# Kernel tuning notes

Hardware: AMD Instinct MI355X
Metric: run time of the kernel (lower is better)

Reference implementation:

```python
import jax, jax.numpy as jnp
import numpy as np

N_NODES = 100000
N_EDGES = 3200000
IN_C, HID_C, OUT_C = 5, 128, 64


def setup_inputs() -> dict:
    key = jax.random.key(0)
    k_x, k_e, k_w1, k_b1, k_w2, k_b2 = jax.random.split(key, 6)
    x = jax.random.normal(k_x, (N_NODES, IN_C), dtype=jnp.float32)
    edge_index = jax.random.randint(k_e, (2, N_EDGES), 0, N_NODES, dtype=jnp.int32)
    # GCNConv learned params (glorot weights, zero-ish bias)
    W1 = jax.random.normal(k_w1, (IN_C, HID_C), dtype=jnp.float32) * (1.0 / np.sqrt(IN_C))
    b1 = jax.random.normal(k_b1, (HID_C,), dtype=jnp.float32) * 0.01
    W2 = jax.random.normal(k_w2, (HID_C, OUT_C), dtype=jnp.float32) * (1.0 / np.sqrt(HID_C))
    b2 = jax.random.normal(k_b2, (OUT_C,), dtype=jnp.float32) * 0.01
    return {"x": x, "edge_index": edge_index, "W1": W1, "b1": b1, "W2": W2, "b2": b2}


def _gcn_conv(x, src, dst, deg_inv_sqrt, W, b):
    """One GCNConv (PyG defaults: self-loops already in src/dst, symmetric norm, bias)."""
    h = x @ W                                   # [N, C_out]
    norm = deg_inv_sqrt[src] * deg_inv_sqrt[dst]  # [E+N]
    msg = h[src] * norm[:, None]                # gather + scale
    out = jax.ops.segment_sum(msg, dst, num_segments=x.shape[0])  # scatter-add
    return out + b


def reference(x, edge_index, W1, b1, W2, b2):
    n = x.shape[0]
    loop = jnp.arange(n, dtype=edge_index.dtype)
    src = jnp.concatenate([edge_index[0], loop])  # self-loops appended
    dst = jnp.concatenate([edge_index[1], loop])
    deg = jax.ops.segment_sum(jnp.ones_like(src, dtype=x.dtype), dst, num_segments=n)
    deg_inv_sqrt = jnp.where(deg > 0, jax.lax.rsqrt(deg), 0.0)
    h = _gcn_conv(x, src, dst, deg_inv_sqrt, W1, b1)
    z = _gcn_conv(h, src, dst, deg_inv_sqrt, W2, b2)
    return z
```

## Files before the change

### kernel.cpp

```cpp
#include <hip/hip_runtime.h>

#define IN_C  5
#define HID_C 128
#define OUT_C 64

#define KB   256
#define NBP  512
#define CAP  10240
#define TILE 8192
#define BTH  512
#define EPT  (TILE / BTH)
#define EPTV (TILE / BTH / 4)
#define GNODES 64

typedef int      vi4 __attribute__((ext_vector_type(4)));
typedef float    vf4 __attribute__((ext_vector_type(4)));
typedef _Float16 vh8 __attribute__((ext_vector_type(8)));


__global__ __launch_bounds__(BTH) void k_bin(const int* __restrict__ src,
                                             const int* __restrict__ dstp,
                                             int* __restrict__ gcursor,
                                             int* __restrict__ binned, int e) {
    __shared__ int lhist[NBP];
    __shared__ int lgofs[NBP];
    __shared__ int lbeg[NBP];
    __shared__ int lsort[TILE];
    __shared__ int gdst[TILE];
    __shared__ int wsum[8];
    __shared__ int stot;
    int tid = threadIdx.x;
    int lane = tid & 63, w = tid >> 6;
    int tbeg = blockIdx.x * TILE;
    lhist[tid] = 0;
    __syncthreads();
    int pk[EPT], bk[EPT], rk[EPT];
    #pragma unroll
    for (int q = 0; q < EPTV; ++q) {
        int idx = tbeg + (q * BTH + tid) * 4;
        if (idx < e) {
            vi4 s4 = __builtin_nontemporal_load((const vi4*)(src + idx));
            vi4 d4 = __builtin_nontemporal_load((const vi4*)(dstp + idx));
            pk[q*4+0] = ((d4.x & 255) << 24) | s4.x; bk[q*4+0] = ((unsigned)d4.x) >> 8;
            pk[q*4+1] = ((d4.y & 255) << 24) | s4.y; bk[q*4+1] = ((unsigned)d4.y) >> 8;
            pk[q*4+2] = ((d4.z & 255) << 24) | s4.z; bk[q*4+2] = ((unsigned)d4.z) >> 8;
            pk[q*4+3] = ((d4.w & 255) << 24) | s4.w; bk[q*4+3] = ((unsigned)d4.w) >> 8;
            rk[q*4+0] = atomicAdd(&lhist[bk[q*4+0]], 1);
            rk[q*4+1] = atomicAdd(&lhist[bk[q*4+1]], 1);
            rk[q*4+2] = atomicAdd(&lhist[bk[q*4+2]], 1);
            rk[q*4+3] = atomicAdd(&lhist[bk[q*4+3]], 1);
        } else {
            bk[q*4+0] = -1; bk[q*4+1] = -1; bk[q*4+2] = -1; bk[q*4+3] = -1;
        }
    }
    __syncthreads();
    int h = lhist[tid];
    int v = h;
    #pragma unroll
    for (int m = 1; m < 64; m <<= 1) { int u = __shfl_up(v, m); if (lane >= m) v += u; }
    if (lane == 63) wsum[w] = v;
    __syncthreads();
    if (tid == 0) {
        int s = 0;
        #pragma unroll
        for (int k = 0; k < 8; ++k) { int tv = wsum[k]; wsum[k] = s; s += tv; }
    }
    __syncthreads();
    int excl = wsum[w] + v - h;
    lbeg[tid] = excl;
    if (h > 0)
        lgofs[tid] = tid * CAP + atomicAdd(&gcursor[tid], h) - excl;
    if (tid == BTH - 1) stot = excl + h;
    __syncthreads();
    #pragma unroll
    for (int q = 0; q < EPT; ++q) {
        if (bk[q] >= 0) {
            int slot = lbeg[bk[q]] + rk[q];
            lsort[slot] = pk[q];
            gdst[slot] = lgofs[bk[q]] + slot;
        }
    }
    __syncthreads();
    int tot = stot;
    for (int i = tid; i < tot; i += BTH)
        binned[gdst[i]] = lsort[i];
}

__global__ __launch_bounds__(BTH) void k_build(int* __restrict__ binned,
                                               const int* __restrict__ gcursor,
                                               const float* __restrict__ x,
                                               int2* __restrict__ pse,
                                               _Float16* __restrict__ xs, int n) {
    __shared__ int cnt[KB];
    __shared__ int wt[4];
    __shared__ int wte[4];
    __shared__ int stage[CAP];
    int tid = threadIdx.x;
    int lane = tid & 63, w = tid >> 6;
    int bkt = blockIdx.x;
    int beg = bkt * CAP;
    int tot = gcursor[bkt];
    if (tid < KB) cnt[tid] = 0;
    __syncthreads();
    int4 r[5];
    int4 rr[5];
    #pragma unroll
    for (int it = 0; it < 5; ++it) {
        int j0 = (tid << 2) + it * (BTH * 4);
        if (j0 < tot) {
            r[it] = *(const int4*)(binned + beg + j0);
            rr[it].x = atomicAdd(&cnt[((unsigned)r[it].x) >> 24], 1);
            if (j0 + 1 < tot) rr[it].y = atomicAdd(&cnt[((unsigned)r[it].y) >> 24], 1);
            if (j0 + 2 < tot) rr[it].z = atomicAdd(&cnt[((unsigned)r[it].z) >> 24], 1);
            if (j0 + 3 < tot) rr[it].w = atomicAdd(&cnt[((unsigned)r[it].w) >> 24], 1);
        }
    }
    __syncthreads();
    int deg = (tid < KB) ? cnt[tid] : 0;
    int v = deg;
    #pragma unroll
    for (int m = 1; m < 64; m <<= 1) { int u = __shfl_up(v, m); if (lane >= m) v += u; }
    if (tid < KB && lane == 63) wt[w] = v;
    __syncthreads();
    if (tid == 0) {
        int s = 0;
        #pragma unroll
        for (int k = 0; k < 4; ++k) { wte[k] = s; s += wt[k]; }
    }
    __syncthreads();
    if (tid < KB) {
        int rel = wte[w] + v - deg;
        int node = bkt * KB + tid;
        pse[node] = make_int2(beg + rel, beg + rel + deg);
        cnt[tid] = rel;
        float d = rsqrtf(1.0f + (float)deg);
        vh8 hq = {};
        if (node < n) {
            hq[0] = (_Float16)(x[node * IN_C + 0] * d);
            hq[1] = (_Float16)(x[node * IN_C + 1] * d);
            hq[2] = (_Float16)(x[node * IN_C + 2] * d);
            hq[3] = (_Float16)(x[node * IN_C + 3] * d);
            hq[4] = (_Float16)(x[node * IN_C + 4] * d);
            hq[5] = (_Float16)d;
        }
        *((vh8*)(xs + (size_t)node * 8)) = hq;
    }
    __syncthreads();
    #pragma unroll
    for (int it = 0; it < 5; ++it) {
        int j0 = (tid << 2) + it * (BTH * 4);
        if (j0 < tot) {
            stage[cnt[((unsigned)r[it].x) >> 24] + rr[it].x] = r[it].x & 0xFFFFFF;
            if (j0 + 1 < tot)
                stage[cnt[((unsigned)r[it].y) >> 24] + rr[it].y] = r[it].y & 0xFFFFFF;
            if (j0 + 2 < tot)
                stage[cnt[((unsigned)r[it].z) >> 24] + rr[it].z] = r[it].z & 0xFFFFFF;
            if (j0 + 3 < tot)
                stage[cnt[((unsigned)r[it].w) >> 24] + rr[it].w] = r[it].w & 0xFFFFFF;
        }
    }
    __syncthreads();
    for (int j = tid; j < tot; j += BTH)
        binned[beg + j] = stage[j];
}

__global__ __launch_bounds__(BTH) void k_gath0(const int* __restrict__ srclist,
                                               const int2* __restrict__ pse,
                                               const _Float16* __restrict__ feat,
                                               _Float16* __restrict__ outf,
                                               float* __restrict__ tout, int n) {
    int tid = threadIdx.x;
    int node = blockIdx.x * GNODES + (tid >> 3);
    int sub = tid & 7;
    if (node >= n) return;
    int2 pp = pse[node];
    int ps = pp.x, pe = pp.y;
    float a0 = 0, a1 = 0, a2 = 0, a3 = 0, a4 = 0, a5 = 0;
    int j = ps + sub;
    for (; j + 24 < pe; j += 32) {
        int s0 = srclist[j],      s1 = srclist[j + 8];
        int s2 = srclist[j + 16], s3 = srclist[j + 24];
        vh8 h0 = *(const vh8*)(feat + (size_t)s0 * 8);
        vh8 h1 = *(const vh8*)(feat + (size_t)s1 * 8);
        vh8 h2 = *(const vh8*)(feat + (size_t)s2 * 8);
        vh8 h3 = *(const vh8*)(feat + (size_t)s3 * 8);
        a0 += ((float)h0[0] + (float)h1[0]) + ((float)h2[0] + (float)h3[0]);
        a1 += ((float)h0[1] + (float)h1[1]) + ((float)h2[1] + (float)h3[1]);
        a2 += ((float)h0[2] + (float)h1[2]) + ((float)h2[2] + (float)h3[2]);
        a3 += ((float)h0[3] + (float)h1[3]) + ((float)h2[3] + (float)h3[3]);
        a4 += ((float)h0[4] + (float)h1[4]) + ((float)h2[4] + (float)h3[4]);
        a5 += ((float)h0[5] + (float)h1[5]) + ((float)h2[5] + (float)h3[5]);
    }
    for (; j < pe; j += 8) {
        int sA = srclist[j];
        vh8 hA = *(const vh8*)(feat + (size_t)sA * 8);
        a0 += (float)hA[0]; a1 += (float)hA[1]; a2 += (float)hA[2];
        a3 += (float)hA[3]; a4 += (float)hA[4]; a5 += (float)hA[5];
    }
    #pragma unroll
    for (int m = 1; m < 8; m <<= 1) {
        a0 += __shfl_xor(a0, m);
        a1 += __shfl_xor(a1, m);
        a2 += __shfl_xor(a2, m);
        a3 += __shfl_xor(a3, m);
        a4 += __shfl_xor(a4, m);
        a5 += __shfl_xor(a5, m);
    }
    if (sub == 0) {
        vh8 hs = *(const vh8*)(feat + (size_t)node * 8);
        float d = (float)hs[5];
        a0 += (float)hs[0]; a1 += (float)hs[1]; a2 += (float)hs[2];
        a3 += (float)hs[3]; a4 += (float)hs[4]; a5 += d;
        float d2 = d * d;
        vh8 ho = {};
        ho[0] = (_Float16)(d2 * a0);
        ho[1] = (_Float16)(d2 * a1);
        ho[2] = (_Float16)(d2 * a2);
        ho[3] = (_Float16)(d2 * a3);
        ho[4] = (_Float16)(d2 * a4);
        ho[5] = (_Float16)d;
        tout[node] = d * a5;
        *((vh8*)(outf + (size_t)node * 8)) = ho;
    }
}

__global__ __launch_bounds__(BTH) void k_gout(const int* __restrict__ srclist,
                                              const int2* __restrict__ pse,
                                              const _Float16* __restrict__ feat,
                                              const float* __restrict__ t,
                                              const float* __restrict__ W1,
                                              const float* __restrict__ b1,
                                              const float* __restrict__ W2,
                                              const float* __restrict__ b2,
                                              float* __restrict__ out, int n) {
    __shared__ float snode[GNODES * 8];
    __shared__ float sW[IN_C * OUT_C + 2 * OUT_C];
    int tid = threadIdx.x;
    if (tid < IN_C * OUT_C) {
        int k = tid >> 6, c = tid & 63;
        float acc = 0.0f;
        for (int m = 0; m < HID_C; ++m)
            acc += W1[k * HID_C + m] * W2[m * OUT_C + c];
        sW[tid] = acc;
    } else if (tid < IN_C * OUT_C + OUT_C) {
        int c = tid - IN_C * OUT_C;
        float acc = 0.0f;
        for (int m = 0; m < HID_C; ++m)
            acc += b1[m] * W2[m * OUT_C + c];
        sW[tid] = acc;
    } else if (tid < IN_C * OUT_C + 2 * OUT_C) {
        sW[tid] = b2[tid - IN_C * OUT_C - OUT_C];
    }
    int node = blockIdx.x * GNODES + (tid >> 3);
    int sub = tid & 7;
    bool act = (node < n);
    float a0 = 0, a1 = 0, a2 = 0, a3 = 0, a4 = 0;
    if (act) {
        int2 pp = pse[node];
        int ps = pp.x, pe = pp.y;
        int j = ps + sub;
        for (; j + 24 < pe; j += 32) {
            int s0 = srclist[j],      s1 = srclist[j + 8];
            int s2 = srclist[j + 16], s3 = srclist[j + 24];
            vh8 h0 = *(const vh8*)(feat + (size_t)s0 * 8);
            vh8 h1 = *(const vh8*)(feat + (size_t)s1 * 8);
            vh8 h2 = *(const vh8*)(feat + (size_t)s2 * 8);
            vh8 h3 = *(const vh8*)(feat + (size_t)s3 * 8);
            a0 += ((float)h0[0] + (float)h1[0]) + ((float)h2[0] + (float)h3[0]);
            a1 += ((float)h0[1] + (float)h1[1]) + ((float)h2[1] + (float)h3[1]);
            a2 += ((float)h0[2] + (float)h1[2]) + ((float)h2[2] + (float)h3[2]);
            a3 += ((float)h0[3] + (float)h1[3]) + ((float)h2[3] + (float)h3[3]);
            a4 += ((float)h0[4] + (float)h1[4]) + ((float)h2[4] + (float)h3[4]);
        }
        for (; j < pe; j += 8) {
            int sA = srclist[j];
            vh8 hA = *(const vh8*)(feat + (size_t)sA * 8);
            a0 += (float)hA[0]; a1 += (float)hA[1]; a2 += (float)hA[2];
            a3 += (float)hA[3]; a4 += (float)hA[4];
        }
    }
    #pragma unroll
    for (int m = 1; m < 8; m <<= 1) {
        a0 += __shfl_xor(a0, m);
        a1 += __shfl_xor(a1, m);
        a2 += __shfl_xor(a2, m);
        a3 += __shfl_xor(a3, m);
        a4 += __shfl_xor(a4, m);
    }
    if (act && sub == 0) {
        vh8 hs = *(const vh8*)(feat + (size_t)node * 8);
        float d = (float)hs[5];
        a0 += (float)hs[0]; a1 += (float)hs[1]; a2 += (float)hs[2];
        a3 += (float)hs[3]; a4 += (float)hs[4];
        float* sn = snode + (tid >> 3) * 8;
        sn[0] = d * a0; sn[1] = d * a1; sn[2] = d * a2;
        sn[3] = d * a3; sn[4] = d * a4; sn[5] = t[node];
    }
    __syncthreads();
    int base = blockIdx.x * GNODES;
    for (int u = tid; u < GNODES * 16; u += BTH) {
        int ln = u >> 4, q = u & 15;
        int i = base + ln;
        if (i >= n) continue;
        const float* a = snode + ln * 8;
        float ti = a[5];
        float4 acc = ((const float4*)(sW + IN_C * OUT_C + OUT_C))[q];
        float4 bq  = ((const float4*)(sW + IN_C * OUT_C))[q];
        acc.x += ti * bq.x; acc.y += ti * bq.y;
        acc.z += ti * bq.z; acc.w += ti * bq.w;
        #pragma unroll
        for (int k = 0; k < IN_C; ++k) {
            float ak = a[k];
            float4 wk = ((const float4*)(sW + k * OUT_C))[q];
            acc.x += ak * wk.x; acc.y += ak * wk.y;
            acc.z += ak * wk.z; acc.w += ak * wk.w;
        }
        vf4 av; av.x = acc.x; av.y = acc.y; av.z = acc.z; av.w = acc.w;
        __builtin_nontemporal_store(av, ((vf4*)out) + (size_t)i * 16 + q);
    }
}

extern "C" void kernel_launch(void* const* d_in, const int* in_sizes, int n_in,
                              void* d_out, int out_size, void* d_ws, size_t ws_size,
                              hipStream_t stream) {
    const float* x   = (const float*)d_in[0];
    const int*   ei  = (const int*)d_in[1];
    const float* W1  = (const float*)d_in[2];
    const float* b1  = (const float*)d_in[3];
    const float* W2  = (const float*)d_in[4];
    const float* b2  = (const float*)d_in[5];
    float* out = (float*)d_out;

    const int n = in_sizes[0] / IN_C;
    const int e = in_sizes[1] / 2;
    const int* src = ei;
    const int* dst = ei + e;
    const int NB = (n + KB - 1) / KB;
    const int NKB = NB * KB;

    int*      gcursor = (int*)d_ws;
    int*      binned  = gcursor + 512;
    int2*     pse     = (int2*)(binned + (size_t)NBP * CAP);
    _Float16* xs      = (_Float16*)(pse + NKB);
    _Float16* p1      = xs + (size_t)8 * NKB;
    float*    t       = (float*)(p1 + (size_t)8 * NKB);

    const int gB = (e + TILE - 1) / TILE;
    const int gG = (n + GNODES - 1) / GNODES;

    (void)hipMemsetAsync(gcursor, 0, NBP * sizeof(int), stream);
    k_bin   <<<gB, BTH, 0, stream>>>(src, dst, gcursor, binned, e);
    k_build <<<NB, BTH, 0, stream>>>(binned, gcursor, x, pse, xs, n);
    k_gath0 <<<gG, BTH, 0, stream>>>(binned, pse, xs, p1, t, n);
    k_gout  <<<gG, BTH, 0, stream>>>(binned, pse, p1, t,
                                     W1, b1, W2, b2, out, n);
}
```

Baseline: 165.9 us.

## Pad per-node edge lists to multiples of four and vectorize index loads

The sort kernel now rounds each node's segment length up to a multiple of four when computing offsets, so every CSR segment starts 16-byte aligned, and it writes the sorted bucket back with int4 stores. Both gather kernels then read four source indices per int4 load, with each of the eight lanes taking contiguous groups of four and the remainder handled in a single tail step. The aim is fewer, wider index loads in the memory-bound gathers, at the cost of padding slots (stage contents at the pads are never read) and relying on the bucket capacity absorbing the extra padding.

```diff
diff --git a/kernel.cpp b/kernel.cpp
--- a/kernel.cpp
+++ b/kernel.cpp
@@ -117,7 +117,8 @@
     }
     __syncthreads();
     int deg = (tid < KB) ? cnt[tid] : 0;
-    int v = deg;
+    int pdeg = (deg + 3) & ~3;
+    int v = pdeg;
     #pragma unroll
     for (int m = 1; m < 64; m <<= 1) { int u = __shfl_up(v, m); if (lane >= m) v += u; }
     if (tid < KB && lane == 63) wt[w] = v;
@@ -129,7 +130,7 @@
     }
     __syncthreads();
     if (tid < KB) {
-        int rel = wte[w] + v - deg;
+        int rel = wte[w] + v - pdeg;
         int node = bkt * KB + tid;
         pse[node] = make_int2(beg + rel, beg + rel + deg);
         cnt[tid] = rel;
@@ -160,8 +161,13 @@
         }
     }
     __syncthreads();
-    for (int j = tid; j < tot; j += BTH)
-        binned[beg + j] = stage[j];
+    int ptot = wte[3] + wt[3];
+    for (int j4 = tid << 2; j4 < ptot; j4 += BTH * 4) {
+        int4 vq;
+        vq.x = stage[j4];     vq.y = stage[j4 + 1];
+        vq.z = stage[j4 + 2]; vq.w = stage[j4 + 3];
+        *(int4*)(binned + beg + j4) = vq;
+    }
 }
 
 __global__ __launch_bounds__(BTH) void k_gath0(const int* __restrict__ srclist,
@@ -175,15 +181,15 @@
     if (node >= n) return;
     int2 pp = pse[node];
     int ps = pp.x, pe = pp.y;
+    int deg = pe - ps;
+    int G = deg >> 2;
     float a0 = 0, a1 = 0, a2 = 0, a3 = 0, a4 = 0, a5 = 0;
-    int j = ps + sub;
-    for (; j + 24 < pe; j += 32) {
-        int s0 = srclist[j],      s1 = srclist[j + 8];
-        int s2 = srclist[j + 16], s3 = srclist[j + 24];
-        vh8 h0 = *(const vh8*)(feat + (size_t)s0 * 8);
-        vh8 h1 = *(const vh8*)(feat + (size_t)s1 * 8);
-        vh8 h2 = *(const vh8*)(feat + (size_t)s2 * 8);
-        vh8 h3 = *(const vh8*)(feat + (size_t)s3 * 8);
+    for (int i = sub; i < G; i += 8) {
+        int4 s4 = *(const int4*)(srclist + ps + (i << 2));
+        vh8 h0 = *(const vh8*)(feat + (size_t)s4.x * 8);
+        vh8 h1 = *(const vh8*)(feat + (size_t)s4.y * 8);
+        vh8 h2 = *(const vh8*)(feat + (size_t)s4.z * 8);
+        vh8 h3 = *(const vh8*)(feat + (size_t)s4.w * 8);
         a0 += ((float)h0[0] + (float)h1[0]) + ((float)h2[0] + (float)h3[0]);
         a1 += ((float)h0[1] + (float)h1[1]) + ((float)h2[1] + (float)h3[1]);
         a2 += ((float)h0[2] + (float)h1[2]) + ((float)h2[2] + (float)h3[2]);
@@ -191,8 +197,8 @@
         a4 += ((float)h0[4] + (float)h1[4]) + ((float)h2[4] + (float)h3[4]);
         a5 += ((float)h0[5] + (float)h1[5]) + ((float)h2[5] + (float)h3[5]);
     }
-    for (; j < pe; j += 8) {
-        int sA = srclist[j];
+    if (sub < (deg & 3)) {
+        int sA = srclist[ps + (G << 2) + sub];
         vh8 hA = *(const vh8*)(feat + (size_t)sA * 8);
         a0 += (float)hA[0]; a1 += (float)hA[1]; a2 += (float)hA[2];
         a3 += (float)hA[3]; a4 += (float)hA[4]; a5 += (float)hA[5];
@@ -258,22 +264,22 @@
     if (act) {
         int2 pp = pse[node];
         int ps = pp.x, pe = pp.y;
-        int j = ps + sub;
-        for (; j + 24 < pe; j += 32) {
-            int s0 = srclist[j],      s1 = srclist[j + 8];
-            int s2 = srclist[j + 16], s3 = srclist[j + 24];
-            vh8 h0 = *(const vh8*)(feat + (size_t)s0 * 8);
-            vh8 h1 = *(const vh8*)(feat + (size_t)s1 * 8);
-            vh8 h2 = *(const vh8*)(feat + (size_t)s2 * 8);
-            vh8 h3 = *(const vh8*)(feat + (size_t)s3 * 8);
+        int deg = pe - ps;
+        int G = deg >> 2;
+        for (int i = sub; i < G; i += 8) {
+            int4 s4 = *(const int4*)(srclist + ps + (i << 2));
+            vh8 h0 = *(const vh8*)(feat + (size_t)s4.x * 8);
+            vh8 h1 = *(const vh8*)(feat + (size_t)s4.y * 8);
+            vh8 h2 = *(const vh8*)(feat + (size_t)s4.z * 8);
+            vh8 h3 = *(const vh8*)(feat + (size_t)s4.w * 8);
             a0 += ((float)h0[0] + (float)h1[0]) + ((float)h2[0] + (float)h3[0]);
             a1 += ((float)h0[1] + (float)h1[1]) + ((float)h2[1] + (float)h3[1]);
             a2 += ((float)h0[2] + (float)h1[2]) + ((float)h2[2] + (float)h3[2]);
             a3 += ((float)h0[3] + (float)h1[3]) + ((float)h2[3] + (float)h3[3]);
             a4 += ((float)h0[4] + (float)h1[4]) + ((float)h2[4] + (float)h3[4]);
         }
-        for (; j < pe; j += 8) {
-            int sA = srclist[j];
+        if (sub < (deg & 3)) {
+            int sA = srclist[ps + (G << 2) + sub];
             vh8 hA = *(const vh8*)(feat + (size_t)sA * 8);
             a0 += (float)hA[0]; a1 += (float)hA[1]; a2 += (float)hA[2];
             a3 += (float)hA[3]; a4 += (float)hA[4];
```

New measurement: 169.9 us. 2.4% more time.
